# Performance work log

Hardware: AMD Instinct MI355X
Metric: run time of the kernel (lower is better)

The kernel has to match this reference:

```python
import jax, jax.numpy as jnp
import numpy as np

NV, NE, NT = 20000, 40000, 30000
D, H, L = 512, 8, 2
HD = D // H
SCALE = float(np.sqrt(HD))
EV, EE, ET = 160000, 160000, 120000
LN_EPS = 1e-5


def _layer_norm(x, g, b):
    m = jnp.mean(x, axis=-1, keepdims=True)
    v = jnp.mean((x - m) ** 2, axis=-1, keepdims=True)
    return (x - m) * jax.lax.rsqrt(v + LN_EPS) * g + b


def _attn_layer(x, ei, W, b, g, bt):
    # x: [N, D]; ei: [2, E]; W: [4, D, D] (q,k,v,out); b: [4, D]
    n = x.shape[0]
    resid = x
    q = (x @ W[0] + b[0]).reshape(n, H, HD)
    k = (x @ W[1] + b[1]).reshape(n, H, HD)
    v = (x @ W[2] + b[2]).reshape(n, H, HD)
    src, dst = ei[0], ei[1]
    # per-edge scores: query at target, key at source (k[edge_index[1]] gather in original)
    scores = jnp.sum(q[dst] * k[src], axis=-1) / SCALE        # [E, H]
    # NOTE: original applies softmax over dim=0, i.e. globally over the edge axis
    w = jax.nn.softmax(scores, axis=0)                         # [E, H]
    msgs = w[:, :, None] * v[src]                              # [E, H, HD]
    out = jax.ops.segment_sum(msgs, dst, num_segments=n)      # [N, H, HD]
    out = out.reshape(n, D) @ W[3] + b[3]
    return _layer_norm(out + resid, g, bt)


def _attn_stack(x, ei, W, b, g, bt):
    for l in range(L):
        x = _attn_layer(x, ei, W[l], b[l], g[l], bt[l])
    return x


def setup_inputs() -> dict:
    key = jax.random.key(0)
    ks = jax.random.split(key, 16)
    inp = {}
    inp['vertices'] = jax.random.normal(ks[0], (NV, D), jnp.float32)
    inp['edge_features'] = jax.random.normal(ks[1], (NE, D), jnp.float32)
    inp['triangle_features'] = jax.random.normal(ks[2], (NT, D), jnp.float32)
    inp['v_embed'] = jax.random.normal(ks[3], (NV, D), jnp.float32)
    inp['e_embed'] = jax.random.normal(ks[4], (NE, D), jnp.float32)
    inp['t_embed'] = jax.random.normal(ks[5], (NT, D), jnp.float32)
    inp['v_pos'] = jax.random.normal(ks[6], (NV, D), jnp.float32) * 0.1
    inp['e_pos'] = jax.random.normal(ks[7], (NE, D), jnp.float32) * 0.1
    inp['t_pos'] = jax.random.normal(ks[8], (NT, D), jnp.float32) * 0.1
    for name, k2 in (('v', ks[9]), ('e', ks[10]), ('t', ks[11])):
        inp[name + 'W'] = jax.random.normal(k2, (L, 4, D, D), jnp.float32) * 0.02
        inp[name + 'B'] = jnp.zeros((L, 4, D), jnp.float32)
        inp[name + 'G'] = jnp.ones((L, D), jnp.float32)
        inp[name + 'Bt'] = jnp.zeros((L, D), jnp.float32)
    inp['head_W'] = jax.random.normal(ks[12], (3, D, D), jnp.float32) * 0.02
    inp['head_b'] = jnp.zeros((3, D), jnp.float32)
    inp['v_ei'] = jax.random.randint(ks[13], (2, EV), 0, NV, jnp.int32)
    inp['e_ei'] = jax.random.randint(ks[14], (2, EE), 0, NE, jnp.int32)
    inp['t_ei'] = jax.random.randint(ks[15], (2, ET), 0, NT, jnp.int32)
    return inp


def reference(vertices, edge_features, triangle_features, v_embed, e_embed, t_embed,
              v_pos, e_pos, t_pos, vW, vB, vG, vBt, eW, eB, eG, eBt,
              tW, tB, tG, tBt, head_W, head_b, v_ei, e_ei, t_ei):
    # embedding(arange(N)) == full table lookup; add positional params and input features
    v = v_embed + v_pos + vertices
    e = e_embed + e_pos + edge_features
    t = t_embed + t_pos + triangle_features
    v = _attn_stack(v, v_ei, vW, vB, vG, vBt)
    e = _attn_stack(e, e_ei, eW, eB, eG, eBt)
    t = _attn_stack(t, t_ei, tW, tB, tG, tBt)
    v_out = v @ head_W[0] + head_b[0]
    e_out = e @ head_W[1] + head_b[1]
    t_out = t @ head_W[2] + head_b[2]
    return (v_out, e_out, t_out)
```

## Files before the change

### kernel.cpp

```cpp
#include <hip/hip_runtime.h>


typedef __attribute__((ext_vector_type(8))) __bf16 bf16x8;
typedef __attribute__((ext_vector_type(4))) float f32x4;
typedef __attribute__((ext_vector_type(8))) unsigned short ushort8v;
typedef __attribute__((ext_vector_type(4))) unsigned short ushort4v;

__device__ __forceinline__ float b2f(unsigned short u) {
  union { unsigned u; float f; } x; x.u = (unsigned)u << 16; return x.f;
}
__device__ __forceinline__ unsigned short f2b(float f) {
  union { float f; unsigned u; } x; x.f = f;
  unsigned r = x.u + 0x7fffu + ((x.u >> 16) & 1u);
  return (unsigned short)(r >> 16);
}

__global__ __launch_bounds__(256) void init_x_kernel(
    const float4* __restrict__ a, const float4* __restrict__ b,
    const float4* __restrict__ c, float4* __restrict__ x,
    unsigned short* __restrict__ xb, long long n4)
{
  long long stride = (long long)gridDim.x * 256;
  for (long long i = (long long)blockIdx.x * 256 + threadIdx.x; i < n4; i += stride) {
    float4 av = a[i], bv = b[i], cv = c[i];
    float4 r;
    r.x = av.x + bv.x + cv.x; r.y = av.y + bv.y + cv.y;
    r.z = av.z + bv.z + cv.z; r.w = av.w + bv.w + cv.w;
    x[i] = r;
    ushort4v o; o.x = f2b(r.x); o.y = f2b(r.y); o.z = f2b(r.z); o.w = f2b(r.w);
    *(ushort4v*)(xb + i * 4) = o;
  }
}

__global__ __launch_bounds__(256) void transpose_w_kernel(
    const float* __restrict__ W, unsigned short* __restrict__ WT)
{
  __shared__ float t[32][33];
  const float* src = W + (size_t)blockIdx.z * 262144;
  unsigned short* dst = WT + (size_t)blockIdx.z * 262144;
  int bx = blockIdx.x * 32, by = blockIdx.y * 32;
  int tx = threadIdx.x, ty = threadIdx.y;
  #pragma unroll
  for (int i = 0; i < 32; i += 8)
    t[ty + i][tx] = src[(size_t)(by + ty + i) * 512 + bx + tx];
  __syncthreads();
  #pragma unroll
  for (int i = 0; i < 32; i += 8) {
    int c = bx + ty + i;
    int p = (c & ~0x3C) | ((c & 0x30) >> 2) | ((c & 0x0C) << 2);
    dst[(size_t)p * 512 + by + tx] = f2b(t[tx][ty + i]);
  }
}

__device__ __forceinline__ void stage16(const void* g, void* lds_uniform) {
  __builtin_amdgcn_global_load_lds(
      (const __attribute__((address_space(1))) void*)g,
      (__attribute__((address_space(3))) void*)lds_uniform, 16, 0, 0);
}

template<int OUT_BF16>
__global__ __launch_bounds__(512, 2) void gemm_bt_kernel(
    const unsigned short* __restrict__ A,
    const unsigned short* __restrict__ BT,
    const float* __restrict__ bias,
    void* __restrict__ Cv,
    int M, int Ncols)
{
  constexpr int K = 512;
  __shared__ unsigned short smem[65536];

  const int nwg = gridDim.x, orig = blockIdx.x;
  const int xcd = orig & 7, lin = orig >> 3;
  const int q = nwg >> 3, r8 = nwg & 7;
  const int wgid = (xcd < r8 ? xcd * (q + 1) : r8 * (q + 1) + (xcd - r8) * q) + lin;

  const int tiles_n = Ncols >> 8;
  const int tm = wgid / tiles_n;
  const int tn = wgid - tm * tiles_n;
  const int row0 = tm << 8, col0 = tn << 8;
  const int lane = threadIdx.x & 63, wid = threadIdx.x >> 6;
  const int wr = (wid >> 2) << 7;
  const int wc = (wid & 3) << 6;

  f32x4 acc[8][4];
  #pragma unroll
  for (int i = 0; i < 8; ++i)
    #pragma unroll
    for (int j = 0; j < 4; ++j) acc[i][j] = (f32x4)0.f;

  int srow[4], scsw[4], sseg[4];
  #pragma unroll
  for (int i = 0; i < 4; ++i) {
    int seg = (i << 3) | wid;
    int idx = (seg << 6) | lane;
    int row = idx >> 3, ch = idx & 7;
    sseg[i] = seg; srow[i] = row; scsw[i] = ch ^ (row & 7);
  }

  #define STG_PAIR(buf, kb_, i)                                               \
    { int ra = row0 + srow[i]; ra = (ra < M) ? ra : (M - 1);                  \
      stage16(A + (size_t)ra * K + (kb_) + (scsw[i] << 3),                    \
              smem + (buf) * 32768 + (sseg[i] << 9));                         \
      int rb = col0 + srow[i];                                                \
      stage16(BT + (size_t)rb * K + (kb_) + (scsw[i] << 3),                   \
              smem + (buf) * 32768 + 16384 + (sseg[i] << 9)); }

  STG_PAIR(0, 0, 0) STG_PAIR(0, 0, 1) STG_PAIR(0, 0, 2) STG_PAIR(0, 0, 3)
  __syncthreads();

  const int lm = lane & 15;
  const int kbl = (lane >> 4) << 4;

  #pragma unroll
  for (int kt = 0; kt < 8; ++kt) {
    const int cur = kt & 1, nxt = cur ^ 1, kb1 = (kt + 1) << 6;
    const char* Asb = (const char*)(smem + cur * 32768);
    const char* Bsb = Asb + 32768;

    auto rdA = [&](int mi, int kk) -> bf16x8 {
      int r = wr + (mi << 4) + lm;
      int kb = (kk << 6) + kbl;
      return *(const bf16x8*)(Asb + (r << 7) + (kb ^ ((r & 7) << 4)));
    };
    auto rdB = [&](int ni, int kk) -> bf16x8 {
      int r = wc + (ni << 4) + lm;
      int kb = (kk << 6) + kbl;
      return *(const bf16x8*)(Bsb + (r << 7) + (kb ^ ((r & 7) << 4)));
    };

    bf16x8 av[4], bv[4];

    #pragma unroll
    for (int i = 0; i < 4; ++i) { av[i] = rdA(i, 0); bv[i] = rdB(i, 0); }
    if (kt < 7) { STG_PAIR(nxt, kb1, 0) STG_PAIR(nxt, kb1, 1) }
    __builtin_amdgcn_s_barrier();
    __builtin_amdgcn_s_setprio(1);
    #pragma unroll
    for (int mi = 0; mi < 4; ++mi)
      #pragma unroll
      for (int ni = 0; ni < 4; ++ni)
        acc[mi][ni] = __builtin_amdgcn_mfma_f32_16x16x32_bf16(
            bv[ni], av[mi], acc[mi][ni], 0, 0, 0);
    __builtin_amdgcn_s_setprio(0);
    __builtin_amdgcn_s_barrier();

    #pragma unroll
    for (int i = 0; i < 4; ++i) av[i] = rdA(4 + i, 0);
    if (kt < 7) { STG_PAIR(nxt, kb1, 2) STG_PAIR(nxt, kb1, 3) }
    __builtin_amdgcn_s_barrier();
    __builtin_amdgcn_s_setprio(1);
    #pragma unroll
    for (int mi = 0; mi < 4; ++mi)
      #pragma unroll
      for (int ni = 0; ni < 4; ++ni)
        acc[4 + mi][ni] = __builtin_amdgcn_mfma_f32_16x16x32_bf16(
            bv[ni], av[mi], acc[4 + mi][ni], 0, 0, 0);
    __builtin_amdgcn_s_setprio(0);
    __builtin_amdgcn_s_barrier();

    #pragma unroll
    for (int i = 0; i < 4; ++i) { av[i] = rdA(i, 1); bv[i] = rdB(i, 1); }
    __builtin_amdgcn_s_barrier();
    __builtin_amdgcn_s_setprio(1);
    #pragma unroll
    for (int mi = 0; mi < 4; ++mi)
      #pragma unroll
      for (int ni = 0; ni < 4; ++ni)
        acc[mi][ni] = __builtin_amdgcn_mfma_f32_16x16x32_bf16(
            bv[ni], av[mi], acc[mi][ni], 0, 0, 0);
    __builtin_amdgcn_s_setprio(0);
    __builtin_amdgcn_s_barrier();

    #pragma unroll
    for (int i = 0; i < 4; ++i) av[i] = rdA(4 + i, 1);
    __builtin_amdgcn_s_barrier();
    __builtin_amdgcn_s_setprio(1);
    #pragma unroll
    for (int mi = 0; mi < 4; ++mi)
      #pragma unroll
      for (int ni = 0; ni < 4; ++ni)
        acc[4 + mi][ni] = __builtin_amdgcn_mfma_f32_16x16x32_bf16(
            bv[ni], av[mi], acc[4 + mi][ni], 0, 0, 0);
    __builtin_amdgcn_s_setprio(0);

    __syncthreads();
  }
  #undef STG_PAIR

  const int mrow = lane & 15;
  const int t4 = (lane >> 4) << 4;
  float bsv[16];
  #pragma unroll
  for (int ni = 0; ni < 4; ++ni) {
    float4 bvv = *(const float4*)(bias + col0 + wc + t4 + (ni << 2));
    bsv[4*ni+0] = bvv.x; bsv[4*ni+1] = bvv.y; bsv[4*ni+2] = bvv.z; bsv[4*ni+3] = bvv.w;
  }

  if (OUT_BF16) {
    unsigned short* C = (unsigned short*)Cv;
    #pragma unroll
    for (int mi = 0; mi < 8; ++mi) {
      int rowg = row0 + wr + (mi << 4) + mrow;
      if (rowg < M) {
        ushort8v o0, o1;
        #pragma unroll
        for (int r = 0; r < 4; ++r) {
          o0[r]     = f2b(acc[mi][0][r] + bsv[r]);
          o0[4 + r] = f2b(acc[mi][1][r] + bsv[4 + r]);
          o1[r]     = f2b(acc[mi][2][r] + bsv[8 + r]);
          o1[4 + r] = f2b(acc[mi][3][r] + bsv[12 + r]);
        }
        unsigned short* cp = C + (size_t)rowg * Ncols + col0 + wc + t4;
        *(ushort8v*)cp = o0;
        *(ushort8v*)(cp + 8) = o1;
      }
    }
  } else {
    float* C = (float*)Cv;
    #pragma unroll
    for (int mi = 0; mi < 8; ++mi) {
      int rowg = row0 + wr + (mi << 4) + mrow;
      if (rowg < M) {
        float* cp = C + (size_t)rowg * Ncols + col0 + wc + t4;
        #pragma unroll
        for (int ni = 0; ni < 4; ++ni) {
          float4 v;
          v.x = acc[mi][ni][0] + bsv[4*ni+0];
          v.y = acc[mi][ni][1] + bsv[4*ni+1];
          v.z = acc[mi][ni][2] + bsv[4*ni+2];
          v.w = acc[mi][ni][3] + bsv[4*ni+3];
          *(float4*)(cp + (ni << 2)) = v;
        }
      }
    }
  }
}

__global__ __launch_bounds__(256) void csr_scores_kernel(
    const unsigned short* __restrict__ qkv, const int* __restrict__ srcs,
    const int* __restrict__ rowptr, int N, float* __restrict__ sc)
{
  int wid = threadIdx.x >> 6, lane = threadIdx.x & 63;
  int n = (blockIdx.x << 2) | wid;
  if (n >= N) return;
  int beg = rowptr[n], end = rowptr[n + 1];
  if (beg == end) return;
  ushort8v qv = *(const ushort8v*)(qkv + (size_t)n * 1536 + (lane << 3));
  float qf[8];
  #pragma unroll
  for (int j = 0; j < 8; ++j) qf[j] = b2f(qv[j]);
  int i = beg;
  for (; i + 2 <= end; i += 2) {
    int s0 = srcs[i], s1 = srcs[i + 1];
    ushort8v k0 = *(const ushort8v*)(qkv + (size_t)s0 * 1536 + 512 + (lane << 3));
    ushort8v k1 = *(const ushort8v*)(qkv + (size_t)s1 * 1536 + 512 + (lane << 3));
    float p0 = 0.f, p1 = 0.f;
    #pragma unroll
    for (int j = 0; j < 8; ++j) { p0 += qf[j] * b2f(k0[j]); p1 += qf[j] * b2f(k1[j]); }
    p0 += __shfl_xor(p0, 1); p1 += __shfl_xor(p1, 1);
    p0 += __shfl_xor(p0, 2); p1 += __shfl_xor(p1, 2);
    p0 += __shfl_xor(p0, 4); p1 += __shfl_xor(p1, 4);
    if (!(lane & 7)) {
      sc[(size_t)i * 8 + (lane >> 3)] = p0 * 0.125f;
      sc[(size_t)(i + 1) * 8 + (lane >> 3)] = p1 * 0.125f;
    }
  }
  if (i < end) {
    int s0 = srcs[i];
    ushort8v k0 = *(const ushort8v*)(qkv + (size_t)s0 * 1536 + 512 + (lane << 3));
    float p0 = 0.f;
    #pragma unroll
    for (int j = 0; j < 8; ++j) p0 += qf[j] * b2f(k0[j]);
    p0 += __shfl_xor(p0, 1);
    p0 += __shfl_xor(p0, 2);
    p0 += __shfl_xor(p0, 4);
    if (!(lane & 7)) sc[(size_t)i * 8 + (lane >> 3)] = p0 * 0.125f;
  }
}

template<int OP>
__device__ __forceinline__ void reduce8_block(float (&v)[8], float* red) {
  int lane = threadIdx.x & 63, wid = threadIdx.x >> 6;
  #pragma unroll
  for (int h = 0; h < 8; ++h)
    #pragma unroll
    for (int off = 1; off < 64; off <<= 1) {
      float o = __shfl_xor(v[h], off);
      v[h] = OP ? (v[h] + o) : fmaxf(v[h], o);
    }
  if (lane == 0) {
    #pragma unroll
    for (int h = 0; h < 8; ++h) red[h * 4 + wid] = v[h];
  }
  __syncthreads();
  if (threadIdx.x == 0) {
    #pragma unroll
    for (int h = 0; h < 8; ++h) {
      float r = red[h * 4];
      #pragma unroll
      for (int w = 1; w < 4; ++w)
        r = OP ? (r + red[h * 4 + w]) : fmaxf(r, red[h * 4 + w]);
      v[h] = r;
    }
  }
}

__global__ __launch_bounds__(256) void sm_max_partial_kernel(
    const float* __restrict__ sc, int E, float* __restrict__ part)
{
  __shared__ float red[32];
  float v[8];
  #pragma unroll
  for (int h = 0; h < 8; ++h) v[h] = -1e30f;
  int stride = gridDim.x * 256;
  for (int e = blockIdx.x * 256 + threadIdx.x; e < E; e += stride) {
    #pragma unroll
    for (int h = 0; h < 8; ++h) v[h] = fmaxf(v[h], sc[(size_t)e * 8 + h]);
  }
  reduce8_block<0>(v, red);
  if (threadIdx.x == 0) {
    #pragma unroll
    for (int h = 0; h < 8; ++h) part[blockIdx.x * 8 + h] = v[h];
  }
}

__global__ __launch_bounds__(256) void sm_exp_partial_kernel(
    float* __restrict__ sc, int E, const float* __restrict__ partm,
    float* __restrict__ parts)
{
  __shared__ float red[32];
  __shared__ float gmx[8];
  float v[8];
  #pragma unroll
  for (int h = 0; h < 8; ++h) v[h] = partm[threadIdx.x * 8 + h];
  reduce8_block<0>(v, red);
  if (threadIdx.x == 0) {
    #pragma unroll
    for (int h = 0; h < 8; ++h) gmx[h] = v[h];
  }
  __syncthreads();
  float gm[8];
  #pragma unroll
  for (int h = 0; h < 8; ++h) { gm[h] = gmx[h]; v[h] = 0.f; }
  int stride = gridDim.x * 256;
  for (int e = blockIdx.x * 256 + threadIdx.x; e < E; e += stride) {
    #pragma unroll
    for (int h = 0; h < 8; ++h) {
      float w = __expf(sc[(size_t)e * 8 + h] - gm[h]);
      sc[(size_t)e * 8 + h] = w;
      v[h] += w;
    }
  }
  reduce8_block<1>(v, red);
  if (threadIdx.x == 0) {
    #pragma unroll
    for (int h = 0; h < 8; ++h) parts[blockIdx.x * 8 + h] = v[h];
  }
}

template<int OP>
__global__ __launch_bounds__(256) void sm_final_kernel(
    const float* __restrict__ part, float* __restrict__ out)
{
  __shared__ float red[32];
  float v[8];
  #pragma unroll
  for (int h = 0; h < 8; ++h) v[h] = part[threadIdx.x * 8 + h];
  reduce8_block<OP>(v, red);
  if (threadIdx.x == 0) {
    #pragma unroll
    for (int h = 0; h < 8; ++h) out[h] = OP ? (1.0f / v[h]) : v[h];
  }
}

__global__ __launch_bounds__(256) void hist_kernel(
    const int* __restrict__ ei, int E, int* __restrict__ deg)
{
  int e = blockIdx.x * 256 + threadIdx.x;
  if (e < E) atomicAdd(&deg[ei[E + e]], 1);
}

__global__ __launch_bounds__(1024) void scan_part_kernel(
    const int* __restrict__ deg, int N, int* __restrict__ rowptr,
    int* __restrict__ bsums)
{
  __shared__ int wsum[16];
  int i = blockIdx.x * 1024 + threadIdx.x;
  int lane = threadIdx.x & 63, wid = threadIdx.x >> 6;
  int sv = (i < N) ? deg[i] : 0;
  #pragma unroll
  for (int off = 1; off < 64; off <<= 1) {
    int t = __shfl_up(sv, off);
    if (lane >= off) sv += t;
  }
  if (lane == 63) wsum[wid] = sv;
  __syncthreads();
  if (threadIdx.x < 16) {
    int ws = wsum[threadIdx.x];
    #pragma unroll
    for (int off = 1; off < 16; off <<= 1) {
      int t = __shfl_up(ws, off);
      if (threadIdx.x >= off) ws += t;
    }
    wsum[threadIdx.x] = ws;
  }
  __syncthreads();
  if (wid > 0) sv += wsum[wid - 1];
  if (i < N) rowptr[i + 1] = sv;
  if (threadIdx.x == 1023) bsums[blockIdx.x] = sv;
}

__global__ __launch_bounds__(64) void scan_bsums_kernel(int* bsums, int nb)
{
  int lane = threadIdx.x;
  int v = (lane < nb) ? bsums[lane] : 0;
  #pragma unroll
  for (int off = 1; off < 64; off <<= 1) {
    int t = __shfl_up(v, off);
    if (lane >= off) v += t;
  }
  int ex = __shfl_up(v, 1);
  if (lane == 0) ex = 0;
  if (lane < nb) bsums[lane] = ex;
}

__global__ __launch_bounds__(1024) void scan_add_kernel(
    int* __restrict__ rowptr, const int* __restrict__ bsums, int N)
{
  int i = blockIdx.x * 1024 + threadIdx.x;
  if (i == 0) rowptr[0] = 0;
  if (i < N && blockIdx.x > 0) rowptr[i + 1] += bsums[blockIdx.x];
}

__global__ __launch_bounds__(256) void scatter_kernel(
    const int* __restrict__ ei, int E, const int* __restrict__ rowptr,
    int* __restrict__ cur, int* __restrict__ srcs)
{
  int e = blockIdx.x * 256 + threadIdx.x;
  if (e < E) {
    int dst = ei[E + e];
    int pos = atomicAdd(&cur[dst], 1);
    srcs[rowptr[dst] + pos] = ei[e];
  }
}

__global__ __launch_bounds__(256) void aggregate_kernel(
    const unsigned short* __restrict__ qkv, const float* __restrict__ wexp,
    const float* __restrict__ ginv, const int* __restrict__ srcs,
    const int* __restrict__ rowptr, int N, unsigned short* __restrict__ agg)
{
  int wid = threadIdx.x >> 6, lane = threadIdx.x & 63;
  int n = (blockIdx.x << 2) | wid;
  if (n >= N) return;
  int beg = rowptr[n], end = rowptr[n + 1];
  int h = lane >> 3;
  float inv = ginv[h];
  float acc[8] = {0.f,0.f,0.f,0.f,0.f,0.f,0.f,0.f};
  int i = beg;
  for (; i + 2 <= end; i += 2) {
    int s0 = srcs[i], s1 = srcs[i + 1];
    float w0 = wexp[(size_t)i * 8 + h] * inv;
    float w1 = wexp[(size_t)(i + 1) * 8 + h] * inv;
    ushort8v v0 = *(const ushort8v*)(qkv + (size_t)s0 * 1536 + 1024 + (lane << 3));
    ushort8v v1 = *(const ushort8v*)(qkv + (size_t)s1 * 1536 + 1024 + (lane << 3));
    #pragma unroll
    for (int j = 0; j < 8; ++j) acc[j] += w0 * b2f(v0[j]) + w1 * b2f(v1[j]);
  }
  if (i < end) {
    int s0 = srcs[i];
    float w0 = wexp[(size_t)i * 8 + h] * inv;
    ushort8v v0 = *(const ushort8v*)(qkv + (size_t)s0 * 1536 + 1024 + (lane << 3));
    #pragma unroll
    for (int j = 0; j < 8; ++j) acc[j] += w0 * b2f(v0[j]);
  }
  ushort8v o;
  #pragma unroll
  for (int j = 0; j < 8; ++j) o[j] = f2b(acc[j]);
  *(ushort8v*)(agg + (size_t)n * 512 + (lane << 3)) = o;
}

__global__ __launch_bounds__(256) void ln_kernel(
    const unsigned short* __restrict__ proj, const float* __restrict__ g,
    const float* __restrict__ bt, float* __restrict__ x,
    unsigned short* __restrict__ xb, int N)
{
  int wid = threadIdx.x >> 6, lane = threadIdx.x & 63;
  int n = (blockIdx.x << 2) | wid;
  if (n >= N) return;
  size_t base = (size_t)n * 512 + (lane << 3);
  ushort8v pv = *(const ushort8v*)(proj + base);
  const float4* xp = (const float4*)(x + base);
  float4 x0 = xp[0], x1 = xp[1];
  float y[8] = {b2f(pv[0]) + x0.x, b2f(pv[1]) + x0.y, b2f(pv[2]) + x0.z,
                b2f(pv[3]) + x0.w, b2f(pv[4]) + x1.x, b2f(pv[5]) + x1.y,
                b2f(pv[6]) + x1.z, b2f(pv[7]) + x1.w};
  float s = 0.f;
  #pragma unroll
  for (int j = 0; j < 8; ++j) s += y[j];
  #pragma unroll
  for (int off = 1; off < 64; off <<= 1) s += __shfl_xor(s, off);
  float mean = s * (1.f / 512.f);
  float vs = 0.f;
  #pragma unroll
  for (int j = 0; j < 8; ++j) { float d = y[j] - mean; vs += d * d; }
  #pragma unroll
  for (int off = 1; off < 64; off <<= 1) vs += __shfl_xor(vs, off);
  float rstd = rsqrtf(vs * (1.f / 512.f) + 1e-5f);
  int gi = lane << 3;
  float o[8];
  #pragma unroll
  for (int j = 0; j < 8; ++j) o[j] = (y[j] - mean) * rstd * g[gi + j] + bt[gi + j];
  float4 r0 = {o[0], o[1], o[2], o[3]}, r1 = {o[4], o[5], o[6], o[7]};
  *(float4*)(x + base) = r0;
  *(float4*)(x + base + 4) = r1;
  ushort8v ob;
  #pragma unroll
  for (int j = 0; j < 8; ++j) ob[j] = f2b(o[j]);
  *(ushort8v*)(xb + base) = ob;
}

extern "C" void kernel_launch(void* const* d_in, const int* in_sizes, int n_in,
                              void* d_out, int out_size, void* d_ws, size_t ws_size,
                              hipStream_t stream)
{
  (void)n_in; (void)out_size;
  const float* feat[3] = {(const float*)d_in[0], (const float*)d_in[1], (const float*)d_in[2]};
  const float* emb[3]  = {(const float*)d_in[3], (const float*)d_in[4], (const float*)d_in[5]};
  const float* pos[3]  = {(const float*)d_in[6], (const float*)d_in[7], (const float*)d_in[8]};
  const float* W[3]  = {(const float*)d_in[9],  (const float*)d_in[13], (const float*)d_in[17]};
  const float* Bb[3] = {(const float*)d_in[10], (const float*)d_in[14], (const float*)d_in[18]};
  const float* G[3]  = {(const float*)d_in[11], (const float*)d_in[15], (const float*)d_in[19]};
  const float* Bt[3] = {(const float*)d_in[12], (const float*)d_in[16], (const float*)d_in[20]};
  const float* headW = (const float*)d_in[21];
  const float* headB = (const float*)d_in[22];
  const int* ei[3] = {(const int*)d_in[23], (const int*)d_in[24], (const int*)d_in[25]};

  int Ns[3], Es[3];
  for (int s = 0; s < 3; ++s) { Ns[s] = in_sizes[s] / 512; Es[s] = in_sizes[23 + s] / 2; }
  int NMAX = Ns[0], EMAX = Es[0];
  for (int s = 1; s < 3; ++s) { if (Ns[s] > NMAX) NMAX = Ns[s]; if (Es[s] > EMAX) EMAX = Es[s]; }

  char* base = (char*)d_ws;
  size_t off = 0;
  auto carve = [&](size_t bytes) -> char* {
    char* r = base + off;
    off += (bytes + 255) & ~(size_t)255;
    return r;
  };
  unsigned short* WT  = (unsigned short*)carve((size_t)27 * 262144 * 2);
  float*          X   = (float*)carve((size_t)NMAX * 512 * 4);
  unsigned short* XB  = (unsigned short*)carve((size_t)NMAX * 512 * 2);
  unsigned short* QKV = (unsigned short*)carve((size_t)NMAX * 1536 * 2);
  float*          SC  = (float*)carve((size_t)EMAX * 8 * 4);
  unsigned short* AGG = (unsigned short*)carve((size_t)NMAX * 512 * 2);
  int*   ROWPTR = (int*)carve((size_t)(NMAX + 1) * 4);
  int*   DEG    = (int*)carve((size_t)NMAX * 4);
  int*   SRCS   = (int*)carve((size_t)EMAX * 4);
  int*   BSUMS  = (int*)carve(64 * 4);
  float* PARTM  = (float*)carve(256 * 8 * 4);
  float* PARTS  = (float*)carve(256 * 8 * 4);
  float* GINV   = (float*)carve(256);
  unsigned short* PROJ = QKV;
  if (off > ws_size) return;

  transpose_w_kernel<<<dim3(16,16,8), dim3(32,8), 0, stream>>>(W[0], WT);
  transpose_w_kernel<<<dim3(16,16,8), dim3(32,8), 0, stream>>>(W[1], WT + (size_t)8 * 262144);
  transpose_w_kernel<<<dim3(16,16,8), dim3(32,8), 0, stream>>>(W[2], WT + (size_t)16 * 262144);
  transpose_w_kernel<<<dim3(16,16,3), dim3(32,8), 0, stream>>>(headW, WT + (size_t)24 * 262144);

  size_t out_off = 0;
  for (int s = 0; s < 3; ++s) {
    const int N = Ns[s], E = Es[s];
    const int mt = (N + 255) >> 8;
    const int nb = (N + 1023) / 1024;

    init_x_kernel<<<2048, 256, 0, stream>>>(
        (const float4*)feat[s], (const float4*)emb[s], (const float4*)pos[s],
        (float4*)X, XB, (long long)N * 128);

    hipMemsetAsync(DEG, 0, (size_t)N * 4, stream);
    hist_kernel<<<(E + 255) / 256, 256, 0, stream>>>(ei[s], E, DEG);
    scan_part_kernel<<<nb, 1024, 0, stream>>>(DEG, N, ROWPTR, BSUMS);
    scan_bsums_kernel<<<1, 64, 0, stream>>>(BSUMS, nb);
    scan_add_kernel<<<nb, 1024, 0, stream>>>(ROWPTR, BSUMS, N);
    hipMemsetAsync(DEG, 0, (size_t)N * 4, stream);
    scatter_kernel<<<(E + 255) / 256, 256, 0, stream>>>(ei[s], E, ROWPTR, DEG, SRCS);

    for (int l = 0; l < 2; ++l) {
      const unsigned short* Wqkv = WT + (size_t)(s * 8 + l * 4) * 262144;
      const unsigned short* Wo   = WT + (size_t)(s * 8 + l * 4 + 3) * 262144;
      const float* bqkv = Bb[s] + (size_t)l * 4 * 512;
      const float* bo   = Bb[s] + (size_t)(l * 4 + 3) * 512;

      gemm_bt_kernel<1><<<dim3(mt * 6), 512, 0, stream>>>(XB, Wqkv, bqkv, QKV, N, 1536);
      csr_scores_kernel<<<(N + 3) / 4, 256, 0, stream>>>(QKV, SRCS, ROWPTR, N, SC);
      sm_max_partial_kernel<<<256, 256, 0, stream>>>(SC, E, PARTM);
      sm_exp_partial_kernel<<<256, 256, 0, stream>>>(SC, E, PARTM, PARTS);
      sm_final_kernel<1><<<1, 256, 0, stream>>>(PARTS, GINV);
      aggregate_kernel<<<(N + 3) / 4, 256, 0, stream>>>(QKV, SC, GINV, SRCS, ROWPTR, N, AGG);
      gemm_bt_kernel<1><<<dim3(mt * 2), 512, 0, stream>>>(AGG, Wo, bo, PROJ, N, 512);
      ln_kernel<<<(N + 3) / 4, 256, 0, stream>>>(PROJ, G[s] + (size_t)l * 512,
                                                 Bt[s] + (size_t)l * 512, X, XB, N);
    }

    gemm_bt_kernel<0><<<dim3(mt * 2), 512, 0, stream>>>(
        XB, WT + (size_t)(24 + s) * 262144, headB + (size_t)s * 512,
        (float*)d_out + out_off, N, 512);
    out_off += (size_t)N * 512;
  }
}
```

Measured before the change: 1.496 ms.

## Drop fp32 residual copy, fuse score max into scores kernel, restructure GEMM k-loop

Removes the fp32 residual buffer X, so init and layer norm now read and write only the bf16 activations. This cuts global traffic but keeps the residual in bf16, which loses precision. The per-edge score kernel now also writes a per-node-wave max, so a small single-block kernel replaces the full pass over scores for the softmax max. The GEMM k-loop is merged into two phases that load all 8 A fragments at once, trading more registers for fewer barriers. The aggregate loop is unrolled to four edges per iteration to keep more gathers in flight.

```diff
diff --git a/kernel.cpp b/kernel.cpp
--- a/kernel.cpp
+++ b/kernel.cpp
@@ -17,17 +17,15 @@
 
 __global__ __launch_bounds__(256) void init_x_kernel(
     const float4* __restrict__ a, const float4* __restrict__ b,
-    const float4* __restrict__ c, float4* __restrict__ x,
-    unsigned short* __restrict__ xb, long long n4)
+    const float4* __restrict__ c, unsigned short* __restrict__ xb,
+    long long n4)
 {
   long long stride = (long long)gridDim.x * 256;
   for (long long i = (long long)blockIdx.x * 256 + threadIdx.x; i < n4; i += stride) {
     float4 av = a[i], bv = b[i], cv = c[i];
-    float4 r;
-    r.x = av.x + bv.x + cv.x; r.y = av.y + bv.y + cv.y;
-    r.z = av.z + bv.z + cv.z; r.w = av.w + bv.w + cv.w;
-    x[i] = r;
-    ushort4v o; o.x = f2b(r.x); o.y = f2b(r.y); o.z = f2b(r.z); o.w = f2b(r.w);
+    ushort4v o;
+    o.x = f2b(av.x + bv.x + cv.x); o.y = f2b(av.y + bv.y + cv.y);
+    o.z = f2b(av.z + bv.z + cv.z); o.w = f2b(av.w + bv.w + cv.w);
     *(ushort4v*)(xb + i * 4) = o;
   }
 }
@@ -128,15 +126,17 @@
       return *(const bf16x8*)(Bsb + (r << 7) + (kb ^ ((r & 7) << 4)));
     };
 
-    bf16x8 av[4], bv[4];
-
-    #pragma unroll
-    for (int i = 0; i < 4; ++i) { av[i] = rdA(i, 0); bv[i] = rdB(i, 0); }
+    bf16x8 av[8], bv[4];
+
+    #pragma unroll
+    for (int i = 0; i < 8; ++i) av[i] = rdA(i, 0);
+    #pragma unroll
+    for (int i = 0; i < 4; ++i) bv[i] = rdB(i, 0);
     if (kt < 7) { STG_PAIR(nxt, kb1, 0) STG_PAIR(nxt, kb1, 1) }
     __builtin_amdgcn_s_barrier();
     __builtin_amdgcn_s_setprio(1);
     #pragma unroll
-    for (int mi = 0; mi < 4; ++mi)
+    for (int mi = 0; mi < 8; ++mi)
       #pragma unroll
       for (int ni = 0; ni < 4; ++ni)
         acc[mi][ni] = __builtin_amdgcn_mfma_f32_16x16x32_bf16(
@@ -145,42 +145,18 @@
     __builtin_amdgcn_s_barrier();
 
     #pragma unroll
-    for (int i = 0; i < 4; ++i) av[i] = rdA(4 + i, 0);
+    for (int i = 0; i < 8; ++i) av[i] = rdA(i, 1);
+    #pragma unroll
+    for (int i = 0; i < 4; ++i) bv[i] = rdB(i, 1);
     if (kt < 7) { STG_PAIR(nxt, kb1, 2) STG_PAIR(nxt, kb1, 3) }
     __builtin_amdgcn_s_barrier();
     __builtin_amdgcn_s_setprio(1);
     #pragma unroll
-    for (int mi = 0; mi < 4; ++mi)
-      #pragma unroll
-      for (int ni = 0; ni < 4; ++ni)
-        acc[4 + mi][ni] = __builtin_amdgcn_mfma_f32_16x16x32_bf16(
-            bv[ni], av[mi], acc[4 + mi][ni], 0, 0, 0);
-    __builtin_amdgcn_s_setprio(0);
-    __builtin_amdgcn_s_barrier();
-
-    #pragma unroll
-    for (int i = 0; i < 4; ++i) { av[i] = rdA(i, 1); bv[i] = rdB(i, 1); }
-    __builtin_amdgcn_s_barrier();
-    __builtin_amdgcn_s_setprio(1);
-    #pragma unroll
-    for (int mi = 0; mi < 4; ++mi)
+    for (int mi = 0; mi < 8; ++mi)
       #pragma unroll
       for (int ni = 0; ni < 4; ++ni)
         acc[mi][ni] = __builtin_amdgcn_mfma_f32_16x16x32_bf16(
             bv[ni], av[mi], acc[mi][ni], 0, 0, 0);
-    __builtin_amdgcn_s_setprio(0);
-    __builtin_amdgcn_s_barrier();
-
-    #pragma unroll
-    for (int i = 0; i < 4; ++i) av[i] = rdA(4 + i, 1);
-    __builtin_amdgcn_s_barrier();
-    __builtin_amdgcn_s_setprio(1);
-    #pragma unroll
-    for (int mi = 0; mi < 4; ++mi)
-      #pragma unroll
-      for (int ni = 0; ni < 4; ++ni)
-        acc[4 + mi][ni] = __builtin_amdgcn_mfma_f32_16x16x32_bf16(
-            bv[ni], av[mi], acc[4 + mi][ni], 0, 0, 0);
     __builtin_amdgcn_s_setprio(0);
 
     __syncthreads();
@@ -238,44 +214,54 @@
 
 __global__ __launch_bounds__(256) void csr_scores_kernel(
     const unsigned short* __restrict__ qkv, const int* __restrict__ srcs,
-    const int* __restrict__ rowptr, int N, float* __restrict__ sc)
+    const int* __restrict__ rowptr, int N, float* __restrict__ sc,
+    float* __restrict__ partm)
 {
   int wid = threadIdx.x >> 6, lane = threadIdx.x & 63;
   int n = (blockIdx.x << 2) | wid;
-  if (n >= N) return;
-  int beg = rowptr[n], end = rowptr[n + 1];
-  if (beg == end) return;
-  ushort8v qv = *(const ushort8v*)(qkv + (size_t)n * 1536 + (lane << 3));
-  float qf[8];
-  #pragma unroll
-  for (int j = 0; j < 8; ++j) qf[j] = b2f(qv[j]);
-  int i = beg;
-  for (; i + 2 <= end; i += 2) {
-    int s0 = srcs[i], s1 = srcs[i + 1];
-    ushort8v k0 = *(const ushort8v*)(qkv + (size_t)s0 * 1536 + 512 + (lane << 3));
-    ushort8v k1 = *(const ushort8v*)(qkv + (size_t)s1 * 1536 + 512 + (lane << 3));
-    float p0 = 0.f, p1 = 0.f;
-    #pragma unroll
-    for (int j = 0; j < 8; ++j) { p0 += qf[j] * b2f(k0[j]); p1 += qf[j] * b2f(k1[j]); }
-    p0 += __shfl_xor(p0, 1); p1 += __shfl_xor(p1, 1);
-    p0 += __shfl_xor(p0, 2); p1 += __shfl_xor(p1, 2);
-    p0 += __shfl_xor(p0, 4); p1 += __shfl_xor(p1, 4);
-    if (!(lane & 7)) {
-      sc[(size_t)i * 8 + (lane >> 3)] = p0 * 0.125f;
-      sc[(size_t)(i + 1) * 8 + (lane >> 3)] = p1 * 0.125f;
-    }
-  }
-  if (i < end) {
-    int s0 = srcs[i];
-    ushort8v k0 = *(const ushort8v*)(qkv + (size_t)s0 * 1536 + 512 + (lane << 3));
-    float p0 = 0.f;
-    #pragma unroll
-    for (int j = 0; j < 8; ++j) p0 += qf[j] * b2f(k0[j]);
-    p0 += __shfl_xor(p0, 1);
-    p0 += __shfl_xor(p0, 2);
-    p0 += __shfl_xor(p0, 4);
-    if (!(lane & 7)) sc[(size_t)i * 8 + (lane >> 3)] = p0 * 0.125f;
-  }
+  float mx = -1e30f;
+  if (n < N) {
+    int beg = rowptr[n], end = rowptr[n + 1];
+    if (beg < end) {
+      ushort8v qv = *(const ushort8v*)(qkv + (size_t)n * 1536 + (lane << 3));
+      float qf[8];
+      #pragma unroll
+      for (int j = 0; j < 8; ++j) qf[j] = b2f(qv[j]);
+      int i = beg;
+      for (; i + 2 <= end; i += 2) {
+        int s0 = srcs[i], s1 = srcs[i + 1];
+        ushort8v k0 = *(const ushort8v*)(qkv + (size_t)s0 * 1536 + 512 + (lane << 3));
+        ushort8v k1 = *(const ushort8v*)(qkv + (size_t)s1 * 1536 + 512 + (lane << 3));
+        float p0 = 0.f, p1 = 0.f;
+        #pragma unroll
+        for (int j = 0; j < 8; ++j) { p0 += qf[j] * b2f(k0[j]); p1 += qf[j] * b2f(k1[j]); }
+        p0 += __shfl_xor(p0, 1); p1 += __shfl_xor(p1, 1);
+        p0 += __shfl_xor(p0, 2); p1 += __shfl_xor(p1, 2);
+        p0 += __shfl_xor(p0, 4); p1 += __shfl_xor(p1, 4);
+        p0 *= 0.125f; p1 *= 0.125f;
+        mx = fmaxf(mx, fmaxf(p0, p1));
+        if (!(lane & 7)) {
+          sc[(size_t)i * 8 + (lane >> 3)] = p0;
+          sc[(size_t)(i + 1) * 8 + (lane >> 3)] = p1;
+        }
+      }
+      if (i < end) {
+        int s0 = srcs[i];
+        ushort8v k0 = *(const ushort8v*)(qkv + (size_t)s0 * 1536 + 512 + (lane << 3));
+        float p0 = 0.f;
+        #pragma unroll
+        for (int j = 0; j < 8; ++j) p0 += qf[j] * b2f(k0[j]);
+        p0 += __shfl_xor(p0, 1);
+        p0 += __shfl_xor(p0, 2);
+        p0 += __shfl_xor(p0, 4);
+        p0 *= 0.125f;
+        mx = fmaxf(mx, p0);
+        if (!(lane & 7)) sc[(size_t)i * 8 + (lane >> 3)] = p0;
+      }
+    }
+  }
+  if (!(lane & 7))
+    partm[(((size_t)blockIdx.x << 2) | wid) * 8 + (lane >> 3)] = mx;
 }
 
 template<int OP>
@@ -305,43 +291,32 @@
   }
 }
 
-__global__ __launch_bounds__(256) void sm_max_partial_kernel(
-    const float* __restrict__ sc, int E, float* __restrict__ part)
+__global__ __launch_bounds__(256) void gmax_kernel(
+    const float* __restrict__ partm, int nslots, float* __restrict__ gmax)
 {
   __shared__ float red[32];
   float v[8];
   #pragma unroll
   for (int h = 0; h < 8; ++h) v[h] = -1e30f;
-  int stride = gridDim.x * 256;
-  for (int e = blockIdx.x * 256 + threadIdx.x; e < E; e += stride) {
-    #pragma unroll
-    for (int h = 0; h < 8; ++h) v[h] = fmaxf(v[h], sc[(size_t)e * 8 + h]);
+  for (int i = threadIdx.x; i < nslots; i += 256) {
+    #pragma unroll
+    for (int h = 0; h < 8; ++h) v[h] = fmaxf(v[h], partm[(size_t)i * 8 + h]);
   }
   reduce8_block<0>(v, red);
   if (threadIdx.x == 0) {
     #pragma unroll
-    for (int h = 0; h < 8; ++h) part[blockIdx.x * 8 + h] = v[h];
+    for (int h = 0; h < 8; ++h) gmax[h] = v[h];
   }
 }
 
 __global__ __launch_bounds__(256) void sm_exp_partial_kernel(
-    float* __restrict__ sc, int E, const float* __restrict__ partm,
+    float* __restrict__ sc, int E, const float* __restrict__ gmax,
     float* __restrict__ parts)
 {
   __shared__ float red[32];
-  __shared__ float gmx[8];
-  float v[8];
-  #pragma unroll
-  for (int h = 0; h < 8; ++h) v[h] = partm[threadIdx.x * 8 + h];
-  reduce8_block<0>(v, red);
-  if (threadIdx.x == 0) {
-    #pragma unroll
-    for (int h = 0; h < 8; ++h) gmx[h] = v[h];
-  }
-  __syncthreads();
-  float gm[8];
-  #pragma unroll
-  for (int h = 0; h < 8; ++h) { gm[h] = gmx[h]; v[h] = 0.f; }
+  float gm[8], v[8];
+  #pragma unroll
+  for (int h = 0; h < 8; ++h) { gm[h] = gmax[h]; v[h] = 0.f; }
   int stride = gridDim.x * 256;
   for (int e = blockIdx.x * 256 + threadIdx.x; e < E; e += stride) {
     #pragma unroll
@@ -457,16 +432,22 @@
   float inv = ginv[h];
   float acc[8] = {0.f,0.f,0.f,0.f,0.f,0.f,0.f,0.f};
   int i = beg;
-  for (; i + 2 <= end; i += 2) {
-    int s0 = srcs[i], s1 = srcs[i + 1];
+  for (; i + 4 <= end; i += 4) {
+    int s0 = srcs[i], s1 = srcs[i + 1], s2 = srcs[i + 2], s3 = srcs[i + 3];
     float w0 = wexp[(size_t)i * 8 + h] * inv;
     float w1 = wexp[(size_t)(i + 1) * 8 + h] * inv;
+    float w2 = wexp[(size_t)(i + 2) * 8 + h] * inv;
+    float w3 = wexp[(size_t)(i + 3) * 8 + h] * inv;
     ushort8v v0 = *(const ushort8v*)(qkv + (size_t)s0 * 1536 + 1024 + (lane << 3));
     ushort8v v1 = *(const ushort8v*)(qkv + (size_t)s1 * 1536 + 1024 + (lane << 3));
-    #pragma unroll
-    for (int j = 0; j < 8; ++j) acc[j] += w0 * b2f(v0[j]) + w1 * b2f(v1[j]);
-  }
-  if (i < end) {
+    ushort8v v2 = *(const ushort8v*)(qkv + (size_t)s2 * 1536 + 1024 + (lane << 3));
+    ushort8v v3 = *(const ushort8v*)(qkv + (size_t)s3 * 1536 + 1024 + (lane << 3));
+    #pragma unroll
+    for (int j = 0; j < 8; ++j)
+      acc[j] += (w0 * b2f(v0[j]) + w1 * b2f(v1[j]))
+              + (w2 * b2f(v2[j]) + w3 * b2f(v3[j]));
+  }
+  for (; i < end; ++i) {
     int s0 = srcs[i];
     float w0 = wexp[(size_t)i * 8 + h] * inv;
     ushort8v v0 = *(const ushort8v*)(qkv + (size_t)s0 * 1536 + 1024 + (lane << 3));
@@ -481,19 +462,17 @@
 
 __global__ __launch_bounds__(256) void ln_kernel(
     const unsigned short* __restrict__ proj, const float* __restrict__ g,
-    const float* __restrict__ bt, float* __restrict__ x,
-    unsigned short* __restrict__ xb, int N)
+    const float* __restrict__ bt, unsigned short* __restrict__ xb, int N)
 {
   int wid = threadIdx.x >> 6, lane = threadIdx.x & 63;
   int n = (blockIdx.x << 2) | wid;
   if (n >= N) return;
   size_t base = (size_t)n * 512 + (lane << 3);
   ushort8v pv = *(const ushort8v*)(proj + base);
-  const float4* xp = (const float4*)(x + base);
-  float4 x0 = xp[0], x1 = xp[1];
-  float y[8] = {b2f(pv[0]) + x0.x, b2f(pv[1]) + x0.y, b2f(pv[2]) + x0.z,
-                b2f(pv[3]) + x0.w, b2f(pv[4]) + x1.x, b2f(pv[5]) + x1.y,
-                b2f(pv[6]) + x1.z, b2f(pv[7]) + x1.w};
+  ushort8v xv = *(const ushort8v*)(xb + base);
+  float y[8];
+  #pragma unroll
+  for (int j = 0; j < 8; ++j) y[j] = b2f(pv[j]) + b2f(xv[j]);
   float s = 0.f;
   #pragma unroll
   for (int j = 0; j < 8; ++j) s += y[j];
@@ -507,15 +486,10 @@
   for (int off = 1; off < 64; off <<= 1) vs += __shfl_xor(vs, off);
   float rstd = rsqrtf(vs * (1.f / 512.f) + 1e-5f);
   int gi = lane << 3;
-  float o[8];
-  #pragma unroll
-  for (int j = 0; j < 8; ++j) o[j] = (y[j] - mean) * rstd * g[gi + j] + bt[gi + j];
-  float4 r0 = {o[0], o[1], o[2], o[3]}, r1 = {o[4], o[5], o[6], o[7]};
-  *(float4*)(x + base) = r0;
-  *(float4*)(x + base + 4) = r1;
   ushort8v ob;
   #pragma unroll
-  for (int j = 0; j < 8; ++j) ob[j] = f2b(o[j]);
+  for (int j = 0; j < 8; ++j)
+    ob[j] = f2b((y[j] - mean) * rstd * g[gi + j] + bt[gi + j]);
   *(ushort8v*)(xb + base) = ob;
 }
 
@@ -548,7 +522,6 @@
     return r;
   };
   unsigned short* WT  = (unsigned short*)carve((size_t)27 * 262144 * 2);
-  float*          X   = (float*)carve((size_t)NMAX * 512 * 4);
   unsigned short* XB  = (unsigned short*)carve((size_t)NMAX * 512 * 2);
   unsigned short* QKV = (unsigned short*)carve((size_t)NMAX * 1536 * 2);
   float*          SC  = (float*)carve((size_t)EMAX * 8 * 4);
@@ -557,8 +530,9 @@
   int*   DEG    = (int*)carve((size_t)NMAX * 4);
   int*   SRCS   = (int*)carve((size_t)EMAX * 4);
   int*   BSUMS  = (int*)carve(64 * 4);
-  float* PARTM  = (float*)carve(256 * 8 * 4);
+  float* PARTM  = (float*)carve((size_t)(NMAX + 8) * 8 * 4);
   float* PARTS  = (float*)carve(256 * 8 * 4);
+  float* GMAX   = (float*)carve(256);
   float* GINV   = (float*)carve(256);
   unsigned short* PROJ = QKV;
   if (off > ws_size) return;
@@ -573,10 +547,11 @@
     const int N = Ns[s], E = Es[s];
     const int mt = (N + 255) >> 8;
     const int nb = (N + 1023) / 1024;
+    const int nsb = (N + 3) / 4;
 
     init_x_kernel<<<2048, 256, 0, stream>>>(
         (const float4*)feat[s], (const float4*)emb[s], (const float4*)pos[s],
-        (float4*)X, XB, (long long)N * 128);
+        XB, (long long)N * 128);
 
     hipMemsetAsync(DEG, 0, (size_t)N * 4, stream);
     hist_kernel<<<(E + 255) / 256, 256, 0, stream>>>(ei[s], E, DEG);
@@ -593,14 +568,14 @@
       const float* bo   = Bb[s] + (size_t)(l * 4 + 3) * 512;
 
       gemm_bt_kernel<1><<<dim3(mt * 6), 512, 0, stream>>>(XB, Wqkv, bqkv, QKV, N, 1536);
-      csr_scores_kernel<<<(N + 3) / 4, 256, 0, stream>>>(QKV, SRCS, ROWPTR, N, SC);
-      sm_max_partial_kernel<<<256, 256, 0, stream>>>(SC, E, PARTM);
-      sm_exp_partial_kernel<<<256, 256, 0, stream>>>(SC, E, PARTM, PARTS);
+      csr_scores_kernel<<<nsb, 256, 0, stream>>>(QKV, SRCS, ROWPTR, N, SC, PARTM);
+      gmax_kernel<<<1, 256, 0, stream>>>(PARTM, nsb * 4, GMAX);
+      sm_exp_partial_kernel<<<256, 256, 0, stream>>>(SC, E, GMAX, PARTS);
       sm_final_kernel<1><<<1, 256, 0, stream>>>(PARTS, GINV);
-      aggregate_kernel<<<(N + 3) / 4, 256, 0, stream>>>(QKV, SC, GINV, SRCS, ROWPTR, N, AGG);
+      aggregate_kernel<<<nsb, 256, 0, stream>>>(QKV, SC, GINV, SRCS, ROWPTR, N, AGG);
       gemm_bt_kernel<1><<<dim3(mt * 2), 512, 0, stream>>>(AGG, Wo, bo, PROJ, N, 512);
-      ln_kernel<<<(N + 3) / 4, 256, 0, stream>>>(PROJ, G[s] + (size_t)l * 512,
-                                                 Bt[s] + (size_t)l * 512, X, XB, N);
+      ln_kernel<<<nsb, 256, 0, stream>>>(PROJ, G[s] + (size_t)l * 512,
+                                         Bt[s] + (size_t)l * 512, XB, N);
     }
 
     gemm_bt_kernel<0><<<dim3(mt * 2), 512, 0, stream>>>(
```

After: 1.544 ms. 1.03x slower.
